# Kernel optimization log

Measured on AMD Instinct MI355X. Metric: run time of the kernel, lower is better.

## Reference

```python
import jax, jax.numpy as jnp
import numpy as np

L, B, T, E, H, V = 6, 4, 1024, 768, 12, 32000
FF = 4 * E


def setup_inputs() -> dict:
    key = jax.random.key(0)
    ks = jax.random.split(key, 16)
    n = lambda k, shape: jax.random.normal(k, shape, jnp.float32) * 0.02
    return {
        "idx": jax.random.randint(ks[0], (B, T), 0, V),
        "targets": jax.random.randint(ks[1], (B, T), 0, V),
        "tok_emb": n(ks[2], (V, E)),
        "pos_emb": n(ks[3], (T, E)),  # block_size == T
        "Wq": n(ks[4], (L, E, E)),
        "Wk": n(ks[5], (L, E, E)),
        "Wv": n(ks[6], (L, E, E)),
        "Wp": n(ks[7], (L, E, E)),
        "bp": jnp.zeros((L, E), jnp.float32),
        "W1": n(ks[8], (L, E, FF)),
        "b1": jnp.zeros((L, FF), jnp.float32),
        "W2": n(ks[9], (L, FF, E)),
        "b2": jnp.zeros((L, E), jnp.float32),
        "ln1_g": jnp.ones((L, E), jnp.float32),
        "ln1_b": jnp.zeros((L, E), jnp.float32),
        "ln2_g": jnp.ones((L, E), jnp.float32),
        "ln2_b": jnp.zeros((L, E), jnp.float32),
        "lnf_g": jnp.ones((E,), jnp.float32),
        "lnf_b": jnp.zeros((E,), jnp.float32),
        "Wlm": n(ks[10], (E, V)),
        "blm": jnp.zeros((V,), jnp.float32),
    }


def _ln(x, g, b):
    m = jnp.mean(x, -1, keepdims=True)
    v = jnp.var(x, -1, keepdims=True)
    return (x - m) * jax.lax.rsqrt(v + 1e-5) * g + b


def _attn(x, wq, wk, wv, wp, pb):
    b, t, e = x.shape
    hs = e // H
    q = (x @ wq).reshape(b, t, H, hs).transpose(0, 2, 1, 3)
    k = (x @ wk).reshape(b, t, H, hs).transpose(0, 2, 1, 3)
    v = (x @ wv).reshape(b, t, H, hs).transpose(0, 2, 1, 3)
    s = jnp.einsum('bhqd,bhkd->bhqk', q, k) * (hs ** -0.5)
    mask = jnp.tril(jnp.ones((t, t), bool))
    s = jnp.where(mask, s, -jnp.inf)
    p = jax.nn.softmax(s, axis=-1)  # dropout = identity at eval
    o = jnp.einsum('bhqk,bhkd->bhqd', p, v).transpose(0, 2, 1, 3).reshape(b, t, e)
    return o @ wp + pb


def reference(idx, targets, tok_emb, pos_emb, Wq, Wk, Wv, Wp, bp, W1, b1, W2, b2,
              ln1_g, ln1_b, ln2_g, ln2_b, lnf_g, lnf_b, Wlm, blm):
    x = tok_emb[idx] + pos_emb[:idx.shape[1]]

    def step(x, p):
        wq, wk, wv, wp, pb, w1, pb1, w2, pb2, g1, bb1, g2, bb2 = p
        x = x + _attn(_ln(x, g1, bb1), wq, wk, wv, wp, pb)
        h = _ln(x, g2, bb2)
        x = x + (jax.nn.relu(h @ w1 + pb1) @ w2 + pb2)
        return x, None

    x, _ = jax.lax.scan(step, x, (Wq, Wk, Wv, Wp, bp, W1, b1, W2, b2,
                                  ln1_g, ln1_b, ln2_g, ln2_b))
    x = _ln(x, lnf_g, lnf_b)
    logits = x @ Wlm + blm
    logp = jax.nn.log_softmax(logits, axis=-1)
    loss = -jnp.mean(jnp.take_along_axis(logp, targets[..., None], axis=-1))
    return logits, loss
```

## Files before the change

kernel.cpp:

```cpp
#include <hip/hip_runtime.h>
#include <hip/hip_bf16.h>
#include <math.h>

#define LAYERS 6
#define BB 4
#define TT 1024
#define EE 768
#define HH 12
#define HS 64
#define VV 32000
#define FFD 3072
#define MROWS (BB * TT)
#define QS (3 * EE)
#define KVB 64
#define QBLK 128
#define NPART (VV / 256)

typedef __attribute__((ext_vector_type(8))) short bf16x8_t;
typedef __attribute__((ext_vector_type(4))) float f32x4_t;

__device__ __forceinline__ float wave_sum(float v) {
#pragma unroll
    for (int o = 32; o > 0; o >>= 1) v += __shfl_xor(v, o);
    return v;
}
__device__ __forceinline__ float wave_max(float v) {
#pragma unroll
    for (int o = 32; o > 0; o >>= 1) v = fmaxf(v, __shfl_xor(v, o));
    return v;
}
__device__ __forceinline__ float block_sum256(float v, float* red) {
    v = wave_sum(v);
    int tid = threadIdx.x;
    if ((tid & 63) == 0) red[tid >> 6] = v;
    __syncthreads();
    float r = red[0] + red[1] + red[2] + red[3];
    __syncthreads();
    return r;
}
__device__ __forceinline__ float block_max256(float v, float* red) {
    v = wave_max(v);
    int tid = threadIdx.x;
    if ((tid & 63) == 0) red[tid >> 6] = v;
    __syncthreads();
    float r = fmaxf(fmaxf(red[0], red[1]), fmaxf(red[2], red[3]));
    __syncthreads();
    return r;
}

__device__ __forceinline__ void gload_lds16(const void* g, void* l) {
    __builtin_amdgcn_global_load_lds((const __attribute__((address_space(1))) void*)g,
                                     (__attribute__((address_space(3))) void*)l, 16, 0, 0);
}

__device__ __forceinline__ unsigned pk2bf(float lo, float hi) {
    __hip_bfloat162 h2 = __float22bfloat162_rn(make_float2(lo, hi));
    return *reinterpret_cast<unsigned*>(&h2);
}

__global__ __launch_bounds__(256) void embed_k(const int* __restrict__ idx,
                                               const float* __restrict__ tok,
                                               const float* __restrict__ pos,
                                               float* __restrict__ x) {
    int row = blockIdx.x;
    int t = row & (TT - 1);
    int token = idx[row];
    const float* te = tok + (size_t)token * EE;
    const float* pe = pos + (size_t)t * EE;
    float* xr = x + (size_t)row * EE;
    for (int i = threadIdx.x; i < EE; i += 256) xr[i] = te[i] + pe[i];
}

__global__ __launch_bounds__(256) void ln_k(const float* __restrict__ x,
                                            const float* __restrict__ g,
                                            const float* __restrict__ b,
                                            __hip_bfloat16* __restrict__ out) {
    __shared__ float sr[EE];
    __shared__ float red[4];
    int row = blockIdx.x;
    const float* xr = x + (size_t)row * EE;
    int tid = threadIdx.x;
    float s = 0.f;
    for (int i = tid; i < EE; i += 256) { float v = xr[i]; sr[i] = v; s += v; }
    s = block_sum256(s, red);
    float m = s * (1.0f / EE);
    float vs = 0.f;
    for (int i = tid; i < EE; i += 256) { float d = sr[i] - m; vs += d * d; }
    vs = block_sum256(vs, red);
    float rstd = rsqrtf(vs * (1.0f / EE) + 1e-5f);
    __hip_bfloat16* orow = out + (size_t)row * EE;
    for (int i = tid; i < EE; i += 256)
        orow[i] = __float2bfloat16((sr[i] - m) * rstd * g[i] + b[i]);
}

__global__ __launch_bounds__(256) void tconv_b_k(const float* __restrict__ W,
                                                 __hip_bfloat16* __restrict__ WT,
                                                 int R, int C,
                                                 size_t wstride, size_t tstride) {
    __shared__ float t[32][33];
    const float* Wl = W + (size_t)blockIdx.z * wstride;
    __hip_bfloat16* Tl = WT + (size_t)blockIdx.z * tstride;
    int c0 = blockIdx.x * 32, r0 = blockIdx.y * 32;
    int tx = threadIdx.x & 31, ty = threadIdx.x >> 5;
#pragma unroll
    for (int i = 0; i < 4; ++i)
        t[ty + 8 * i][tx] = Wl[(size_t)(r0 + ty + 8 * i) * C + c0 + tx];
    __syncthreads();
#pragma unroll
    for (int i = 0; i < 4; ++i)
        Tl[(size_t)(c0 + ty + 8 * i) * R + r0 + tx] = __float2bfloat16(t[tx][ty + 8 * i]);
}

template <bool BIAS, bool RELU, bool ACCUM, bool OBF16>
__global__ __launch_bounds__(256) void mgemm_k(const __hip_bfloat16* __restrict__ A,
                                               const __hip_bfloat16* __restrict__ BT,
                                               const float* __restrict__ bias,
                                               void* __restrict__ Cv,
                                               int M, int N, int K, int ntn) {
    __shared__ __align__(16) short As[128 * 32];
    __shared__ __align__(16) short Bs[128 * 32];

    int nwg = gridDim.x;
    int bid = blockIdx.x;
    int cpx = nwg >> 3;
    int swz = (bid & 7) * cpx + (bid >> 3);
    int tm = swz / ntn, tn = swz - tm * ntn;
    int m0 = tm * 128, n0 = tn * 128;

    int tid = threadIdx.x;
    int lane = tid & 63;
    int wave = tid >> 6;
    int wr = wave >> 1, wc = wave & 1;

    f32x4_t acc[4][4];
#pragma unroll
    for (int i = 0; i < 4; ++i)
#pragma unroll
        for (int j = 0; j < 4; ++j)
#pragma unroll
            for (int r = 0; r < 4; ++r) acc[i][j][r] = 0.f;

    const short* Ag = (const short*)A;
    const short* Bg = (const short*)BT;
    const int arow0 = tid >> 2;
    const int arow1 = (tid + 256) >> 2;
    const int acol = (tid & 3) * 8;

    const int fr = lane & 15;
    const int kg = (lane >> 4) * 8;

    for (int k0 = 0; k0 < K; k0 += 32) {
        gload_lds16(Ag + (size_t)(m0 + arow0) * K + k0 + acol, &As[tid * 8]);
        gload_lds16(Ag + (size_t)(m0 + arow1) * K + k0 + acol, &As[(tid + 256) * 8]);
        gload_lds16(Bg + (size_t)(n0 + arow0) * K + k0 + acol, &Bs[tid * 8]);
        gload_lds16(Bg + (size_t)(n0 + arow1) * K + k0 + acol, &Bs[(tid + 256) * 8]);
        __syncthreads();

        bf16x8_t af[4], bq[4];
#pragma unroll
        for (int mi = 0; mi < 4; ++mi)
            af[mi] = *(const bf16x8_t*)&As[(wr * 64 + mi * 16 + fr) * 32 + kg];
#pragma unroll
        for (int ni = 0; ni < 4; ++ni)
            bq[ni] = *(const bf16x8_t*)&Bs[(wc * 64 + ni * 16 + fr) * 32 + kg];
#pragma unroll
        for (int mi = 0; mi < 4; ++mi)
#pragma unroll
            for (int ni = 0; ni < 4; ++ni)
                acc[mi][ni] = __builtin_amdgcn_mfma_f32_16x16x32_bf16(af[mi], bq[ni], acc[mi][ni], 0, 0, 0);
        __syncthreads();
    }

    float bvec[4];
    if (BIAS) {
#pragma unroll
        for (int ni = 0; ni < 4; ++ni) bvec[ni] = bias[n0 + wc * 64 + ni * 16 + fr];
    }
    const int rbase = m0 + wr * 64 + (lane >> 4) * 4;
    const int cbase = n0 + wc * 64 + fr;
#pragma unroll
    for (int mi = 0; mi < 4; ++mi) {
#pragma unroll
        for (int ni = 0; ni < 4; ++ni) {
#pragma unroll
            for (int r = 0; r < 4; ++r) {
                int row = rbase + mi * 16 + r;
                int col = cbase + ni * 16;
                float v = acc[mi][ni][r];
                if (BIAS) v += bvec[ni];
                if (RELU) v = fmaxf(v, 0.f);
                size_t off = (size_t)row * N + col;
                if (OBF16) {
                    ((__hip_bfloat16*)Cv)[off] = __float2bfloat16(v);
                } else {
                    float* Cf = (float*)Cv;
                    if (ACCUM) Cf[off] += v; else Cf[off] = v;
                }
            }
        }
    }
}

__device__ __forceinline__ bf16x8_t ldsrd256(const short* base, int row, int colb) {
    return *(const bf16x8_t*)((const char*)base + ((row << 7) + (colb ^ ((row & 7) << 4))));
}

template <bool BIAS, bool RELU, bool OBF16, bool LSE>
__global__ __launch_bounds__(512, 2) void mgemm256_k(const __hip_bfloat16* __restrict__ A,
                                                     const __hip_bfloat16* __restrict__ BT,
                                                     const float* __restrict__ bias,
                                                     void* __restrict__ Cv,
                                                     int M, int N, int K,
                                                     int ntn, int npart,
                                                     float2* __restrict__ partials) {
    __shared__ __align__(16) short lds[2][2][2][8192];

    const int nwg = gridDim.x;
    const int bid = blockIdx.x;
    const int cpx = nwg >> 3;
    const int swz = (bid & 7) * cpx + (bid >> 3);
    const int tm = swz / ntn, tn = swz - tm * ntn;
    const int m0 = tm * 256, n0 = tn * 256;

    const int tid = threadIdx.x;
    const int lane = tid & 63;
    const int wave = tid >> 6;
    const int wm = wave >> 2;
    const int wn = wave & 3;
    const int fr = lane & 15;
    const int hi4 = lane >> 4;

    const short* Ag = (const short*)A;
    const short* Bg = (const short*)BT;
    const int nt = K >> 6;

    auto stage_half = [&](const short* g, int grow0, int k0, short* lbase) {
#pragma unroll
        for (int sub = 0; sub < 2; ++sub) {
            int d = sub * 8192 + tid * 16;
            int row = d >> 7;
            int cb = d & 127;
            int col = (cb ^ ((row & 7) << 4)) >> 1;
            gload_lds16(g + (size_t)(grow0 + row) * K + k0 + col, (char*)lbase + d);
        }
    };

    f32x4_t acc[2][2][4][2];
#pragma unroll
    for (int ah = 0; ah < 2; ++ah)
#pragma unroll
        for (int s = 0; s < 2; ++s)
#pragma unroll
            for (int mi = 0; mi < 4; ++mi)
#pragma unroll
                for (int ni = 0; ni < 2; ++ni)
#pragma unroll
                    for (int r = 0; r < 4; ++r) acc[ah][s][mi][ni][r] = 0.f;

    stage_half(Ag, m0 + 0,   0,  &lds[0][0][0][0]);
    stage_half(Bg, n0 + 0,   0,  &lds[0][1][0][0]);
    stage_half(Ag, m0 + 128, 0,  &lds[0][0][1][0]);
    stage_half(Bg, n0 + 128, 0,  &lds[0][1][1][0]);
    stage_half(Ag, m0 + 0,   64, &lds[1][0][0][0]);
    stage_half(Bg, n0 + 0,   64, &lds[1][1][0][0]);
    asm volatile("s_waitcnt vmcnt(4)" ::: "memory");
    __builtin_amdgcn_s_barrier();

    for (int t = 0; t < nt; ++t) {
        const int c = t & 1, o = c ^ 1;
        bf16x8_t a[4][2];
#pragma unroll
        for (int p = 0; p < 4; ++p) {
            const int ah = p >> 1, s = p & 1;
            if (s == 0) {
#pragma unroll
                for (int mi = 0; mi < 4; ++mi)
#pragma unroll
                    for (int kk = 0; kk < 2; ++kk)
                        a[mi][kk] = ldsrd256(&lds[c][0][ah][0],
                                             wm * 64 + mi * 16 + fr, kk * 64 + hi4 * 16);
            }
            bf16x8_t b[2][2];
#pragma unroll
            for (int ni = 0; ni < 2; ++ni)
#pragma unroll
                for (int kk = 0; kk < 2; ++kk)
                    b[ni][kk] = ldsrd256(&lds[c][1][s][0],
                                         wn * 32 + ni * 16 + fr, kk * 64 + hi4 * 16);
            if (p == 0 && t + 1 < nt) stage_half(Ag, m0 + 128, (t + 1) * 64, &lds[o][0][1][0]);
            if (p == 1 && t + 1 < nt) stage_half(Bg, n0 + 128, (t + 1) * 64, &lds[o][1][1][0]);
            if (p == 2 && t + 2 < nt) stage_half(Ag, m0 + 0,   (t + 2) * 64, &lds[c][0][0][0]);
            if (p == 3 && t + 2 < nt) stage_half(Bg, n0 + 0,   (t + 2) * 64, &lds[c][1][0][0]);
            if (p == 3) {
                if (t < nt - 2)       asm volatile("s_waitcnt vmcnt(4)" ::: "memory");
                else if (t == nt - 2) asm volatile("s_waitcnt vmcnt(0)" ::: "memory");
            }
            __builtin_amdgcn_s_barrier();
            asm volatile("s_waitcnt lgkmcnt(0)" ::: "memory");
            __builtin_amdgcn_sched_barrier(0);
            __builtin_amdgcn_s_setprio(1);
#pragma unroll
            for (int mi = 0; mi < 4; ++mi)
#pragma unroll
                for (int ni = 0; ni < 2; ++ni)
#pragma unroll
                    for (int kk = 0; kk < 2; ++kk)
                        acc[ah][s][mi][ni] = __builtin_amdgcn_mfma_f32_16x16x32_bf16(
                            a[mi][kk], b[ni][kk], acc[ah][s][mi][ni], 0, 0, 0);
            __builtin_amdgcn_s_setprio(0);
            __builtin_amdgcn_s_barrier();
        }
    }

    float bv[2][2];
    if (BIAS) {
#pragma unroll
        for (int s = 0; s < 2; ++s)
#pragma unroll
            for (int ni = 0; ni < 2; ++ni)
                bv[s][ni] = bias[n0 + s * 128 + wn * 32 + ni * 16 + fr];
    }
    float2* red = (float2*)&lds[0][0][0][0];
#pragma unroll
    for (int ah = 0; ah < 2; ++ah) {
#pragma unroll
        for (int mi = 0; mi < 4; ++mi) {
#pragma unroll
            for (int r = 0; r < 4; ++r) {
                const int rb = ah * 128 + wm * 64 + mi * 16 + hi4 * 4 + r;
                const size_t grow = (size_t)(m0 + rb);
                float v[2][2];
#pragma unroll
                for (int s = 0; s < 2; ++s)
#pragma unroll
                    for (int ni = 0; ni < 2; ++ni) {
                        float vv = acc[ah][s][mi][ni][r];
                        if (BIAS) vv += bv[s][ni];
                        if (RELU) vv = fmaxf(vv, 0.f);
                        v[s][ni] = vv;
                        size_t off = grow * N + n0 + s * 128 + wn * 32 + ni * 16 + fr;
                        if (OBF16) ((__hip_bfloat16*)Cv)[off] = __float2bfloat16(vv);
                        else       ((float*)Cv)[off] = vv;
                    }
                if (LSE) {
                    float mx = fmaxf(fmaxf(v[0][0], v[0][1]), fmaxf(v[1][0], v[1][1]));
#pragma unroll
                    for (int off2 = 1; off2 < 16; off2 <<= 1) mx = fmaxf(mx, __shfl_xor(mx, off2));
                    float sm = 0.f;
#pragma unroll
                    for (int s = 0; s < 2; ++s)
#pragma unroll
                        for (int ni = 0; ni < 2; ++ni) sm += __expf(v[s][ni] - mx);
#pragma unroll
                    for (int off2 = 1; off2 < 16; off2 <<= 1) sm += __shfl_xor(sm, off2);
                    if (fr == 0) red[rb * 4 + wn] = make_float2(mx, sm);
                }
            }
        }
    }
    if (LSE) {
        __syncthreads();
        if (tid < 256) {
            float2 p0 = red[tid * 4 + 0], p1 = red[tid * 4 + 1];
            float2 p2 = red[tid * 4 + 2], p3 = red[tid * 4 + 3];
            float M2 = fmaxf(fmaxf(p0.x, p1.x), fmaxf(p2.x, p3.x));
            float L2 = p0.y * __expf(p0.x - M2) + p1.y * __expf(p1.x - M2) +
                       p2.y * __expf(p2.x - M2) + p3.y * __expf(p3.x - M2);
            partials[(size_t)(m0 + tid) * npart + tn] = make_float2(M2, L2);
        }
    }
}

__global__ __launch_bounds__(256) void fattn_k(const __hip_bfloat16* __restrict__ qkv,
                                               __hip_bfloat16* __restrict__ o) {
    __shared__ short Ks[KVB * HS];
    __shared__ short Vt[HS * KVB];
    __shared__ short Pl[4 * 32 * KVB];

    const int bh = blockIdx.x;
    const int hh = bh % HH;
    const int bI = bh / HH;
    const int qt = (TT / QBLK - 1) - blockIdx.y;
    const int q0 = qt * QBLK;

    const int tid = threadIdx.x;
    const int lane = tid & 63;
    const int wave = tid >> 6;
    const int fr = lane & 15;
    const int hi4 = lane >> 4;

    const size_t rowbase = (size_t)bI * TT;
    const int wq0 = q0 + wave * 32;

    bf16x8_t qf[2][2];
#pragma unroll
    for (int mi = 0; mi < 2; ++mi)
#pragma unroll
        for (int kc = 0; kc < 2; ++kc) {
            const short* src = (const short*)qkv +
                (rowbase + wq0 + mi * 16 + fr) * QS + hh * HS + kc * 32 + hi4 * 8;
            bf16x8_t v = *(const bf16x8_t*)src;
#pragma unroll
            for (int e = 0; e < 8; ++e) {
                float f = __uint_as_float(((unsigned)(unsigned short)v[e]) << 16) * 0.125f;
                v[e] = (short)(__float_as_uint(f) >> 16);
            }
            qf[mi][kc] = v;
        }

    f32x4_t oa[2][4];
    float m_r[2], l_r[2];
#pragma unroll
    for (int mi = 0; mi < 2; ++mi) {
        m_r[mi] = -INFINITY;
        l_r[mi] = 0.f;
#pragma unroll
        for (int nd = 0; nd < 4; ++nd)
#pragma unroll
            for (int r = 0; r < 4; ++r) oa[mi][nd][r] = 0.f;
    }

    const int skey = tid >> 2;
    const int sd0 = (tid & 3) * 16;
    const int niter = 2 * (qt + 1);

    for (int it = 0; it < niter; ++it) {
        const int kv0 = it * KVB;
        __syncthreads();
        {
            const short* kg = (const short*)qkv + (rowbase + kv0 + skey) * QS + EE + hh * HS + sd0;
            uint4 ka = *(const uint4*)kg;
            uint4 kb2 = *(const uint4*)(kg + 8);
            const int rs = (skey & 7) << 4;
            char* kbp = (char*)Ks;
            *(uint4*)(kbp + ((skey * 128 + sd0 * 2) ^ rs)) = ka;
            *(uint4*)(kbp + ((skey * 128 + sd0 * 2 + 16) ^ rs)) = kb2;

            const short* vg = (const short*)qkv + (rowbase + kv0 + skey) * QS + 2 * EE + hh * HS + sd0;
            uint4 va = *(const uint4*)vg;
            uint4 vb2 = *(const uint4*)(vg + 8);
            char* vbp = (char*)Vt;
            const short* vs0 = (const short*)&va;
#pragma unroll
            for (int e = 0; e < 8; ++e) {
                int dd = sd0 + e;
                *(short*)(vbp + ((dd * 128 + skey * 2) ^ ((dd & 7) << 4))) = vs0[e];
            }
            const short* vs1 = (const short*)&vb2;
#pragma unroll
            for (int e = 0; e < 8; ++e) {
                int dd = sd0 + 8 + e;
                *(short*)(vbp + ((dd * 128 + skey * 2) ^ ((dd & 7) << 4))) = vs1[e];
            }
        }
        __syncthreads();

        f32x4_t sa[2][4];
#pragma unroll
        for (int mi = 0; mi < 2; ++mi)
#pragma unroll
            for (int ni = 0; ni < 4; ++ni)
#pragma unroll
                for (int r = 0; r < 4; ++r) sa[mi][ni][r] = 0.f;
#pragma unroll
        for (int kc = 0; kc < 2; ++kc) {
            bf16x8_t kf[4];
#pragma unroll
            for (int ni = 0; ni < 4; ++ni) {
                int krow = ni * 16 + fr;
                kf[ni] = *(const bf16x8_t*)((char*)Ks +
                    ((krow * 128 + (kc * 32 + hi4 * 8) * 2) ^ ((krow & 7) << 4)));
            }
#pragma unroll
            for (int mi = 0; mi < 2; ++mi)
#pragma unroll
                for (int ni = 0; ni < 4; ++ni)
                    sa[mi][ni] = __builtin_amdgcn_mfma_f32_16x16x32_bf16(kf[ni], qf[mi][kc], sa[mi][ni], 0, 0, 0);
        }

        if (kv0 + KVB - 1 > wq0) {
#pragma unroll
            for (int mi = 0; mi < 2; ++mi) {
                int qrow = wq0 + mi * 16 + fr;
#pragma unroll
                for (int ni = 0; ni < 4; ++ni)
#pragma unroll
                    for (int r = 0; r < 4; ++r) {
                        int key = kv0 + ni * 16 + hi4 * 4 + r;
                        if (key > qrow) sa[mi][ni][r] = -1e30f;
                    }
            }
        }

        char* Pw = (char*)Pl + wave * 4096;
#pragma unroll
        for (int mi = 0; mi < 2; ++mi) {
            float mx = sa[mi][0][0];
#pragma unroll
            for (int ni = 0; ni < 4; ++ni)
#pragma unroll
                for (int r = 0; r < 4; ++r) mx = fmaxf(mx, sa[mi][ni][r]);
            mx = fmaxf(mx, __shfl_xor(mx, 16));
            mx = fmaxf(mx, __shfl_xor(mx, 32));
            float mnew = fmaxf(m_r[mi], mx);
            float al = __expf(m_r[mi] - mnew);
            m_r[mi] = mnew;
            float ps = 0.f;
#pragma unroll
            for (int ni = 0; ni < 4; ++ni) {
#pragma unroll
                for (int r = 0; r < 4; ++r) {
                    float p = __expf(sa[mi][ni][r] - mnew);
                    sa[mi][ni][r] = p;
                    ps += p;
                }
                uint2 pw;
                pw.x = pk2bf(sa[mi][ni][0], sa[mi][ni][1]);
                pw.y = pk2bf(sa[mi][ni][2], sa[mi][ni][3]);
                int prow = mi * 16 + fr;
                int cb = ni * 32 + hi4 * 8;
                *(uint2*)(Pw + ((prow * 128 + cb) ^ ((prow & 7) << 4))) = pw;
            }
            ps += __shfl_xor(ps, 16);
            ps += __shfl_xor(ps, 32);
            l_r[mi] = l_r[mi] * al + ps;
#pragma unroll
            for (int r = 0; r < 4; ++r) {
                float a_r = __shfl(al, hi4 * 4 + r);
#pragma unroll
                for (int nd = 0; nd < 4; ++nd) oa[mi][nd][r] *= a_r;
            }
        }

#pragma unroll
        for (int kc = 0; kc < 2; ++kc) {
            bf16x8_t pf[2], vf[4];
#pragma unroll
            for (int mi = 0; mi < 2; ++mi) {
                int prow = mi * 16 + fr;
                pf[mi] = *(const bf16x8_t*)(Pw +
                    ((prow * 128 + (kc * 32 + hi4 * 8) * 2) ^ ((prow & 7) << 4)));
            }
#pragma unroll
            for (int nd = 0; nd < 4; ++nd) {
                int vrow = nd * 16 + fr;
                vf[nd] = *(const bf16x8_t*)((char*)Vt +
                    ((vrow * 128 + (kc * 32 + hi4 * 8) * 2) ^ ((vrow & 7) << 4)));
            }
#pragma unroll
            for (int mi = 0; mi < 2; ++mi)
#pragma unroll
                for (int nd = 0; nd < 4; ++nd)
                    oa[mi][nd] = __builtin_amdgcn_mfma_f32_16x16x32_bf16(pf[mi], vf[nd], oa[mi][nd], 0, 0, 0);
        }
    }

#pragma unroll
    for (int mi = 0; mi < 2; ++mi)
#pragma unroll
        for (int r = 0; r < 4; ++r) {
            float lr = __shfl(l_r[mi], hi4 * 4 + r);
            float inv = 1.0f / lr;
            int row = wq0 + mi * 16 + hi4 * 4 + r;
            __hip_bfloat16* orow = o + (rowbase + row) * EE + hh * HS;
#pragma unroll
            for (int nd = 0; nd < 4; ++nd)
                orow[nd * 16 + fr] = __float2bfloat16(oa[mi][nd][r] * inv);
        }
}

__global__ __launch_bounds__(256) void rowloss2_k(const float2* __restrict__ partials,
                                                  const float* __restrict__ logits,
                                                  const int* __restrict__ targets,
                                                  float* __restrict__ rowloss, int ntn) {
    __shared__ float red[4];
    int row = blockIdx.x;
    int tid = threadIdx.x;
    float m = -INFINITY, l = 0.f;
    if (tid < ntn) {
        float2 p = partials[(size_t)row * ntn + tid];
        m = p.x; l = p.y;
    }
    float mg = block_max256(m, red);
    float s = (tid < ntn) ? l * __expf(m - mg) : 0.f;
    s = block_sum256(s, red);
    if (tid == 0)
        rowloss[row] = mg + logf(s) - logits[(size_t)row * VV + targets[row]];
}

__global__ __launch_bounds__(256) void loss_final_k(const float* __restrict__ rowloss,
                                                    float* __restrict__ out) {
    __shared__ float red[4];
    float s = 0.f;
    for (int i = threadIdx.x; i < MROWS; i += 256) s += rowloss[i];
    s = block_sum256(s, red);
    if (threadIdx.x == 0) out[0] = s * (1.0f / MROWS);
}

extern "C" void kernel_launch(void* const* d_in, const int* in_sizes, int n_in,
                              void* d_out, int out_size, void* d_ws, size_t ws_size,
                              hipStream_t stream) {
    const int* idx      = (const int*)d_in[0];
    const int* targets  = (const int*)d_in[1];
    const float* tok    = (const float*)d_in[2];
    const float* pos    = (const float*)d_in[3];
    const float* Wq     = (const float*)d_in[4];
    const float* Wk     = (const float*)d_in[5];
    const float* Wv     = (const float*)d_in[6];
    const float* Wp     = (const float*)d_in[7];
    const float* bp     = (const float*)d_in[8];
    const float* W1     = (const float*)d_in[9];
    const float* b1     = (const float*)d_in[10];
    const float* W2     = (const float*)d_in[11];
    const float* b2     = (const float*)d_in[12];
    const float* ln1_g  = (const float*)d_in[13];
    const float* ln1_b  = (const float*)d_in[14];
    const float* ln2_g  = (const float*)d_in[15];
    const float* ln2_b  = (const float*)d_in[16];
    const float* lnf_g  = (const float*)d_in[17];
    const float* lnf_b  = (const float*)d_in[18];
    const float* Wlm    = (const float*)d_in[19];
    const float* blm    = (const float*)d_in[20];

    float* out = (float*)d_out;

    char* w = (char*)d_ws;
    float* x = (float*)w;                             w += (size_t)MROWS * EE * 4;
    __hip_bfloat16* hbf = (__hip_bfloat16*)w;         w += (size_t)MROWS * EE * 2;
    __hip_bfloat16* qkv = (__hip_bfloat16*)w;         w += (size_t)MROWS * QS * 2;
    __hip_bfloat16* obf = (__hip_bfloat16*)w;         w += (size_t)MROWS * EE * 2;
    __hip_bfloat16* ff1 = (__hip_bfloat16*)w;         w += (size_t)MROWS * FFD * 2;
    float2* partials = (float2*)ff1;
    __hip_bfloat16* wlmT = (__hip_bfloat16*)w;        w += (size_t)VV * EE * 2;
    float* rowloss = (float*)w;                       w += (size_t)MROWS * 4 + 256;
    __hip_bfloat16* wbase = (__hip_bfloat16*)w;

    const size_t base_used = (size_t)(w - (char*)d_ws);
    const size_t per_layer_w = ((size_t)QS * EE + (size_t)EE * EE +
                                (size_t)FFD * EE + (size_t)EE * FFD) * 2;
    const bool hoist = ws_size >= base_used + per_layer_w * LAYERS;
    const int nlw = hoist ? LAYERS : 1;

    __hip_bfloat16* qkvwT = wbase;
    __hip_bfloat16* wpT   = qkvwT + (size_t)nlw * QS * EE;
    __hip_bfloat16* w1T   = wpT   + (size_t)nlw * EE * EE;
    __hip_bfloat16* w2T   = w1T   + (size_t)nlw * FFD * EE;

    dim3 blk(256);

    embed_k<<<MROWS, blk, 0, stream>>>(idx, tok, pos, x);

    if (hoist) {
        tconv_b_k<<<dim3(EE / 32, EE / 32, LAYERS), blk, 0, stream>>>(
            Wq, qkvwT, EE, EE, (size_t)EE * EE, (size_t)QS * EE);
        tconv_b_k<<<dim3(EE / 32, EE / 32, LAYERS), blk, 0, stream>>>(
            Wk, qkvwT + (size_t)EE * EE, EE, EE, (size_t)EE * EE, (size_t)QS * EE);
        tconv_b_k<<<dim3(EE / 32, EE / 32, LAYERS), blk, 0, stream>>>(
            Wv, qkvwT + (size_t)2 * EE * EE, EE, EE, (size_t)EE * EE, (size_t)QS * EE);
        tconv_b_k<<<dim3(EE / 32, EE / 32, LAYERS), blk, 0, stream>>>(
            Wp, wpT, EE, EE, (size_t)EE * EE, (size_t)EE * EE);
        tconv_b_k<<<dim3(FFD / 32, EE / 32, LAYERS), blk, 0, stream>>>(
            W1, w1T, EE, FFD, (size_t)EE * FFD, (size_t)FFD * EE);
        tconv_b_k<<<dim3(EE / 32, FFD / 32, LAYERS), blk, 0, stream>>>(
            W2, w2T, FFD, EE, (size_t)FFD * EE, (size_t)EE * FFD);
    }
    tconv_b_k<<<dim3(VV / 32, EE / 32, 1), blk, 0, stream>>>(Wlm, wlmT, EE, VV, 0, 0);

    for (int l = 0; l < LAYERS; ++l) {
        __hip_bfloat16* qkvwT_l = qkvwT + (hoist ? (size_t)l * QS * EE : 0);
        __hip_bfloat16* wpT_l   = wpT   + (hoist ? (size_t)l * EE * EE : 0);
        __hip_bfloat16* w1T_l   = w1T   + (hoist ? (size_t)l * FFD * EE : 0);
        __hip_bfloat16* w2T_l   = w2T   + (hoist ? (size_t)l * EE * FFD : 0);
        if (!hoist) {
            tconv_b_k<<<dim3(EE / 32, EE / 32, 1), blk, 0, stream>>>(
                Wq + (size_t)l * EE * EE, qkvwT_l, EE, EE, 0, 0);
            tconv_b_k<<<dim3(EE / 32, EE / 32, 1), blk, 0, stream>>>(
                Wk + (size_t)l * EE * EE, qkvwT_l + (size_t)EE * EE, EE, EE, 0, 0);
            tconv_b_k<<<dim3(EE / 32, EE / 32, 1), blk, 0, stream>>>(
                Wv + (size_t)l * EE * EE, qkvwT_l + (size_t)2 * EE * EE, EE, EE, 0, 0);
            tconv_b_k<<<dim3(EE / 32, EE / 32, 1), blk, 0, stream>>>(
                Wp + (size_t)l * EE * EE, wpT_l, EE, EE, 0, 0);
            tconv_b_k<<<dim3(FFD / 32, EE / 32, 1), blk, 0, stream>>>(
                W1 + (size_t)l * EE * FFD, w1T_l, EE, FFD, 0, 0);
            tconv_b_k<<<dim3(EE / 32, FFD / 32, 1), blk, 0, stream>>>(
                W2 + (size_t)l * FFD * EE, w2T_l, FFD, EE, 0, 0);
        }

        ln_k<<<MROWS, blk, 0, stream>>>(x, ln1_g + l * EE, ln1_b + l * EE, hbf);
        mgemm_k<false, false, false, true><<<dim3((MROWS / 128) * (QS / 128)), blk, 0, stream>>>(
            hbf, qkvwT_l, nullptr, qkv, MROWS, QS, EE, QS / 128);
        fattn_k<<<dim3(BB * HH, TT / QBLK), blk, 0, stream>>>(qkv, obf);
        mgemm_k<true, false, true, false><<<dim3((MROWS / 128) * (EE / 128)), blk, 0, stream>>>(
            obf, wpT_l, bp + l * EE, x, MROWS, EE, EE, EE / 128);
        ln_k<<<MROWS, blk, 0, stream>>>(x, ln2_g + l * EE, ln2_b + l * EE, hbf);
        mgemm_k<true, true, false, true><<<dim3((MROWS / 128) * (FFD / 128)), blk, 0, stream>>>(
            hbf, w1T_l, b1 + l * FFD, ff1, MROWS, FFD, EE, FFD / 128);
        mgemm_k<true, false, true, false><<<dim3((MROWS / 128) * (EE / 128)), blk, 0, stream>>>(
            ff1, w2T_l, b2 + l * EE, x, MROWS, EE, FFD, EE / 128);
    }

    ln_k<<<MROWS, blk, 0, stream>>>(x, lnf_g, lnf_b, hbf);
    mgemm256_k<true, false, false, true><<<dim3((MROWS / 256) * (VV / 256)), dim3(512), 0, stream>>>(
        hbf, wlmT, blm, out, MROWS, VV, EE, VV / 256, NPART, partials);

    rowloss2_k<<<MROWS, blk, 0, stream>>>(partials, out, targets, rowloss, NPART);
    loss_final_k<<<1, blk, 0, stream>>>(rowloss, out + (size_t)MROWS * VV);
}
```

Baseline: 1.850 ms.

## Vectorize embed/layernorm, simplify LM-head GEMM tiling, prefetch K/V in attention

Embedding and layernorm now process four rows per block, one wave per row, with float4 loads and wave-level reductions instead of block reductions through LDS. The LM-head GEMM is replaced by a simpler 128x256 tile kernel with a single LDS buffer and a K step of 32 per barrier pair. It drops the hand-pipelined double buffering and the 256x256 tile in exchange for higher occupancy (launch bounds of 4 blocks per unit). Flash attention now register-prefetches the next K/V tile while computing the current one, hiding global load latency. The LM-head change risks losing the previous software pipelining on the largest GEMM.

```diff
diff --git a/kernel.cpp b/kernel.cpp
--- a/kernel.cpp
+++ b/kernel.cpp
@@ -58,39 +58,62 @@
     return *reinterpret_cast<unsigned*>(&h2);
 }
 
-__global__ __launch_bounds__(256) void embed_k(const int* __restrict__ idx,
-                                               const float* __restrict__ tok,
-                                               const float* __restrict__ pos,
-                                               float* __restrict__ x) {
-    int row = blockIdx.x;
+__global__ __launch_bounds__(256) void embed4_k(const int* __restrict__ idx,
+                                                const float* __restrict__ tok,
+                                                const float* __restrict__ pos,
+                                                float* __restrict__ x) {
+    int row = blockIdx.x * 4 + (threadIdx.x >> 6);
+    int lane = threadIdx.x & 63;
     int t = row & (TT - 1);
     int token = idx[row];
-    const float* te = tok + (size_t)token * EE;
-    const float* pe = pos + (size_t)t * EE;
-    float* xr = x + (size_t)row * EE;
-    for (int i = threadIdx.x; i < EE; i += 256) xr[i] = te[i] + pe[i];
-}
-
-__global__ __launch_bounds__(256) void ln_k(const float* __restrict__ x,
-                                            const float* __restrict__ g,
-                                            const float* __restrict__ b,
-                                            __hip_bfloat16* __restrict__ out) {
-    __shared__ float sr[EE];
-    __shared__ float red[4];
-    int row = blockIdx.x;
-    const float* xr = x + (size_t)row * EE;
-    int tid = threadIdx.x;
+    const float4* te = (const float4*)(tok + (size_t)token * EE);
+    const float4* pe = (const float4*)(pos + (size_t)t * EE);
+    float4* xr = (float4*)(x + (size_t)row * EE);
+#pragma unroll
+    for (int j = 0; j < 3; ++j) {
+        int i = j * 64 + lane;
+        float4 a = te[i], b = pe[i];
+        xr[i] = make_float4(a.x + b.x, a.y + b.y, a.z + b.z, a.w + b.w);
+    }
+}
+
+__global__ __launch_bounds__(256) void ln4_k(const float* __restrict__ x,
+                                             const float* __restrict__ g,
+                                             const float* __restrict__ b,
+                                             __hip_bfloat16* __restrict__ out) {
+    int row = blockIdx.x * 4 + (threadIdx.x >> 6);
+    int lane = threadIdx.x & 63;
+    const float4* xr = (const float4*)(x + (size_t)row * EE);
+    float4 v[3];
     float s = 0.f;
-    for (int i = tid; i < EE; i += 256) { float v = xr[i]; sr[i] = v; s += v; }
-    s = block_sum256(s, red);
+#pragma unroll
+    for (int j = 0; j < 3; ++j) {
+        v[j] = xr[j * 64 + lane];
+        s += v[j].x + v[j].y + v[j].z + v[j].w;
+    }
+    s = wave_sum(s);
     float m = s * (1.0f / EE);
     float vs = 0.f;
-    for (int i = tid; i < EE; i += 256) { float d = sr[i] - m; vs += d * d; }
-    vs = block_sum256(vs, red);
+#pragma unroll
+    for (int j = 0; j < 3; ++j) {
+        float d0 = v[j].x - m, d1 = v[j].y - m, d2 = v[j].z - m, d3 = v[j].w - m;
+        vs += d0 * d0 + d1 * d1 + d2 * d2 + d3 * d3;
+    }
+    vs = wave_sum(vs);
     float rstd = rsqrtf(vs * (1.0f / EE) + 1e-5f);
-    __hip_bfloat16* orow = out + (size_t)row * EE;
-    for (int i = tid; i < EE; i += 256)
-        orow[i] = __float2bfloat16((sr[i] - m) * rstd * g[i] + b[i]);
+    const float4* g4 = (const float4*)g;
+    const float4* b4 = (const float4*)b;
+    uint2* orow = (uint2*)(out + (size_t)row * EE);
+#pragma unroll
+    for (int j = 0; j < 3; ++j) {
+        int i = j * 64 + lane;
+        float4 gg = g4[i], bb = b4[i];
+        float n0 = (v[j].x - m) * rstd * gg.x + bb.x;
+        float n1 = (v[j].y - m) * rstd * gg.y + bb.y;
+        float n2 = (v[j].z - m) * rstd * gg.z + bb.z;
+        float n3 = (v[j].w - m) * rstd * gg.w + bb.w;
+        orow[i] = make_uint2(pk2bf(n0, n1), pk2bf(n2, n3));
+    }
 }
 
 __global__ __launch_bounds__(256) void tconv_b_k(const float* __restrict__ W,
@@ -201,26 +224,22 @@
     }
 }
 
-__device__ __forceinline__ bf16x8_t ldsrd256(const short* base, int row, int colb) {
-    return *(const bf16x8_t*)((const char*)base + ((row << 7) + (colb ^ ((row & 7) << 4))));
-}
-
-template <bool BIAS, bool RELU, bool OBF16, bool LSE>
-__global__ __launch_bounds__(512, 2) void mgemm256_k(const __hip_bfloat16* __restrict__ A,
+__global__ __launch_bounds__(512, 4) void mgemm_lm_k(const __hip_bfloat16* __restrict__ A,
                                                      const __hip_bfloat16* __restrict__ BT,
                                                      const float* __restrict__ bias,
-                                                     void* __restrict__ Cv,
+                                                     float* __restrict__ C,
                                                      int M, int N, int K,
                                                      int ntn, int npart,
                                                      float2* __restrict__ partials) {
-    __shared__ __align__(16) short lds[2][2][2][8192];
+    __shared__ __align__(16) short As[128 * 32];
+    __shared__ __align__(16) short Bs[256 * 32];
 
     const int nwg = gridDim.x;
     const int bid = blockIdx.x;
     const int cpx = nwg >> 3;
     const int swz = (bid & 7) * cpx + (bid >> 3);
     const int tm = swz / ntn, tn = swz - tm * ntn;
-    const int m0 = tm * 256, n0 = tn * 256;
+    const int m0 = tm * 128, n0 = tn * 256;
 
     const int tid = threadIdx.x;
     const int lane = tid & 63;
@@ -230,144 +249,79 @@
     const int fr = lane & 15;
     const int hi4 = lane >> 4;
 
+    f32x4_t acc[4][4];
+#pragma unroll
+    for (int i = 0; i < 4; ++i)
+#pragma unroll
+        for (int j = 0; j < 4; ++j)
+#pragma unroll
+            for (int r = 0; r < 4; ++r) acc[i][j][r] = 0.f;
+
     const short* Ag = (const short*)A;
     const short* Bg = (const short*)BT;
-    const int nt = K >> 6;
-
-    auto stage_half = [&](const short* g, int grow0, int k0, short* lbase) {
-#pragma unroll
-        for (int sub = 0; sub < 2; ++sub) {
-            int d = sub * 8192 + tid * 16;
-            int row = d >> 7;
-            int cb = d & 127;
-            int col = (cb ^ ((row & 7) << 4)) >> 1;
-            gload_lds16(g + (size_t)(grow0 + row) * K + k0 + col, (char*)lbase + d);
-        }
-    };
-
-    f32x4_t acc[2][2][4][2];
-#pragma unroll
-    for (int ah = 0; ah < 2; ++ah)
-#pragma unroll
-        for (int s = 0; s < 2; ++s)
-#pragma unroll
-            for (int mi = 0; mi < 4; ++mi)
-#pragma unroll
-                for (int ni = 0; ni < 2; ++ni)
-#pragma unroll
-                    for (int r = 0; r < 4; ++r) acc[ah][s][mi][ni][r] = 0.f;
-
-    stage_half(Ag, m0 + 0,   0,  &lds[0][0][0][0]);
-    stage_half(Bg, n0 + 0,   0,  &lds[0][1][0][0]);
-    stage_half(Ag, m0 + 128, 0,  &lds[0][0][1][0]);
-    stage_half(Bg, n0 + 128, 0,  &lds[0][1][1][0]);
-    stage_half(Ag, m0 + 0,   64, &lds[1][0][0][0]);
-    stage_half(Bg, n0 + 0,   64, &lds[1][1][0][0]);
-    asm volatile("s_waitcnt vmcnt(4)" ::: "memory");
-    __builtin_amdgcn_s_barrier();
-
-    for (int t = 0; t < nt; ++t) {
-        const int c = t & 1, o = c ^ 1;
-        bf16x8_t a[4][2];
-#pragma unroll
-        for (int p = 0; p < 4; ++p) {
-            const int ah = p >> 1, s = p & 1;
-            if (s == 0) {
-#pragma unroll
-                for (int mi = 0; mi < 4; ++mi)
-#pragma unroll
-                    for (int kk = 0; kk < 2; ++kk)
-                        a[mi][kk] = ldsrd256(&lds[c][0][ah][0],
-                                             wm * 64 + mi * 16 + fr, kk * 64 + hi4 * 16);
-            }
-            bf16x8_t b[2][2];
-#pragma unroll
-            for (int ni = 0; ni < 2; ++ni)
-#pragma unroll
-                for (int kk = 0; kk < 2; ++kk)
-                    b[ni][kk] = ldsrd256(&lds[c][1][s][0],
-                                         wn * 32 + ni * 16 + fr, kk * 64 + hi4 * 16);
-            if (p == 0 && t + 1 < nt) stage_half(Ag, m0 + 128, (t + 1) * 64, &lds[o][0][1][0]);
-            if (p == 1 && t + 1 < nt) stage_half(Bg, n0 + 128, (t + 1) * 64, &lds[o][1][1][0]);
-            if (p == 2 && t + 2 < nt) stage_half(Ag, m0 + 0,   (t + 2) * 64, &lds[c][0][0][0]);
-            if (p == 3 && t + 2 < nt) stage_half(Bg, n0 + 0,   (t + 2) * 64, &lds[c][1][0][0]);
-            if (p == 3) {
-                if (t < nt - 2)       asm volatile("s_waitcnt vmcnt(4)" ::: "memory");
-                else if (t == nt - 2) asm volatile("s_waitcnt vmcnt(0)" ::: "memory");
-            }
-            __builtin_amdgcn_s_barrier();
-            asm volatile("s_waitcnt lgkmcnt(0)" ::: "memory");
-            __builtin_amdgcn_sched_barrier(0);
-            __builtin_amdgcn_s_setprio(1);
-#pragma unroll
-            for (int mi = 0; mi < 4; ++mi)
-#pragma unroll
-                for (int ni = 0; ni < 2; ++ni)
-#pragma unroll
-                    for (int kk = 0; kk < 2; ++kk)
-                        acc[ah][s][mi][ni] = __builtin_amdgcn_mfma_f32_16x16x32_bf16(
-                            a[mi][kk], b[ni][kk], acc[ah][s][mi][ni], 0, 0, 0);
-            __builtin_amdgcn_s_setprio(0);
-            __builtin_amdgcn_s_barrier();
-        }
-    }
-
-    float bv[2][2];
-    if (BIAS) {
-#pragma unroll
-        for (int s = 0; s < 2; ++s)
-#pragma unroll
-            for (int ni = 0; ni < 2; ++ni)
-                bv[s][ni] = bias[n0 + s * 128 + wn * 32 + ni * 16 + fr];
-    }
-    float2* red = (float2*)&lds[0][0][0][0];
-#pragma unroll
-    for (int ah = 0; ah < 2; ++ah) {
-#pragma unroll
-        for (int mi = 0; mi < 4; ++mi) {
-#pragma unroll
-            for (int r = 0; r < 4; ++r) {
-                const int rb = ah * 128 + wm * 64 + mi * 16 + hi4 * 4 + r;
-                const size_t grow = (size_t)(m0 + rb);
-                float v[2][2];
-#pragma unroll
-                for (int s = 0; s < 2; ++s)
-#pragma unroll
-                    for (int ni = 0; ni < 2; ++ni) {
-                        float vv = acc[ah][s][mi][ni][r];
-                        if (BIAS) vv += bv[s][ni];
-                        if (RELU) vv = fmaxf(vv, 0.f);
-                        v[s][ni] = vv;
-                        size_t off = grow * N + n0 + s * 128 + wn * 32 + ni * 16 + fr;
-                        if (OBF16) ((__hip_bfloat16*)Cv)[off] = __float2bfloat16(vv);
-                        else       ((float*)Cv)[off] = vv;
-                    }
-                if (LSE) {
-                    float mx = fmaxf(fmaxf(v[0][0], v[0][1]), fmaxf(v[1][0], v[1][1]));
-#pragma unroll
-                    for (int off2 = 1; off2 < 16; off2 <<= 1) mx = fmaxf(mx, __shfl_xor(mx, off2));
-                    float sm = 0.f;
-#pragma unroll
-                    for (int s = 0; s < 2; ++s)
-#pragma unroll
-                        for (int ni = 0; ni < 2; ++ni) sm += __expf(v[s][ni] - mx);
-#pragma unroll
-                    for (int off2 = 1; off2 < 16; off2 <<= 1) sm += __shfl_xor(sm, off2);
-                    if (fr == 0) red[rb * 4 + wn] = make_float2(mx, sm);
-                }
-            }
-        }
-    }
-    if (LSE) {
+    const int srow = tid >> 2;
+    const int scol = (tid & 3) * 8;
+    const int kg = hi4 * 8;
+
+    for (int k0 = 0; k0 < K; k0 += 32) {
+        gload_lds16(Ag + (size_t)(m0 + srow) * K + k0 + scol, &As[tid * 8]);
+        gload_lds16(Bg + (size_t)(n0 + srow) * K + k0 + scol, &Bs[tid * 8]);
+        gload_lds16(Bg + (size_t)(n0 + 128 + srow) * K + k0 + scol, &Bs[(tid + 512) * 8]);
         __syncthreads();
-        if (tid < 256) {
-            float2 p0 = red[tid * 4 + 0], p1 = red[tid * 4 + 1];
-            float2 p2 = red[tid * 4 + 2], p3 = red[tid * 4 + 3];
-            float M2 = fmaxf(fmaxf(p0.x, p1.x), fmaxf(p2.x, p3.x));
-            float L2 = p0.y * __expf(p0.x - M2) + p1.y * __expf(p1.x - M2) +
-                       p2.y * __expf(p2.x - M2) + p3.y * __expf(p3.x - M2);
-            partials[(size_t)(m0 + tid) * npart + tn] = make_float2(M2, L2);
-        }
+
+        bf16x8_t af[4], bq[4];
+#pragma unroll
+        for (int mi = 0; mi < 4; ++mi)
+            af[mi] = *(const bf16x8_t*)&As[(wm * 64 + mi * 16 + fr) * 32 + kg];
+#pragma unroll
+        for (int ni = 0; ni < 4; ++ni)
+            bq[ni] = *(const bf16x8_t*)&Bs[(wn * 64 + ni * 16 + fr) * 32 + kg];
+#pragma unroll
+        for (int mi = 0; mi < 4; ++mi)
+#pragma unroll
+            for (int ni = 0; ni < 4; ++ni)
+                acc[mi][ni] = __builtin_amdgcn_mfma_f32_16x16x32_bf16(af[mi], bq[ni], acc[mi][ni], 0, 0, 0);
+        __syncthreads();
+    }
+
+    float bvec[4];
+#pragma unroll
+    for (int ni = 0; ni < 4; ++ni) bvec[ni] = bias[n0 + wn * 64 + ni * 16 + fr];
+
+    float2* red = (float2*)As;
+    const int cbase = n0 + wn * 64 + fr;
+#pragma unroll
+    for (int mi = 0; mi < 4; ++mi) {
+#pragma unroll
+        for (int r = 0; r < 4; ++r) {
+            const int rl = wm * 64 + mi * 16 + hi4 * 4 + r;
+            const size_t grow = (size_t)(m0 + rl);
+            float v4[4];
+#pragma unroll
+            for (int ni = 0; ni < 4; ++ni) {
+                float v = acc[mi][ni][r] + bvec[ni];
+                v4[ni] = v;
+                C[grow * N + cbase + ni * 16] = v;
+            }
+            float mx = fmaxf(fmaxf(v4[0], v4[1]), fmaxf(v4[2], v4[3]));
+#pragma unroll
+            for (int o = 1; o < 16; o <<= 1) mx = fmaxf(mx, __shfl_xor(mx, o));
+            float sm = 0.f;
+#pragma unroll
+            for (int ni = 0; ni < 4; ++ni) sm += __expf(v4[ni] - mx);
+#pragma unroll
+            for (int o = 1; o < 16; o <<= 1) sm += __shfl_xor(sm, o);
+            if (fr == 0) red[rl * 4 + wn] = make_float2(mx, sm);
+        }
+    }
+    __syncthreads();
+    if (tid < 128) {
+        float2 p0 = red[tid * 4 + 0], p1 = red[tid * 4 + 1];
+        float2 p2 = red[tid * 4 + 2], p3 = red[tid * 4 + 3];
+        float M2 = fmaxf(fmaxf(p0.x, p1.x), fmaxf(p2.x, p3.x));
+        float L2 = p0.y * __expf(p0.x - M2) + p1.y * __expf(p1.x - M2) +
+                   p2.y * __expf(p2.x - M2) + p3.y * __expf(p3.x - M2);
+        partials[(size_t)(m0 + tid) * npart + tn] = make_float2(M2, L2);
     }
 }
 
@@ -424,21 +378,22 @@
     const int sd0 = (tid & 3) * 16;
     const int niter = 2 * (qt + 1);
 
+    uint4 ka, kb2, va, vb2;
+    {
+        const short* kg = (const short*)qkv + (rowbase + skey) * QS + EE + hh * HS + sd0;
+        ka = *(const uint4*)kg; kb2 = *(const uint4*)(kg + 8);
+        const short* vg = (const short*)qkv + (rowbase + skey) * QS + 2 * EE + hh * HS + sd0;
+        va = *(const uint4*)vg; vb2 = *(const uint4*)(vg + 8);
+    }
+
     for (int it = 0; it < niter; ++it) {
-        const int kv0 = it * KVB;
         __syncthreads();
         {
-            const short* kg = (const short*)qkv + (rowbase + kv0 + skey) * QS + EE + hh * HS + sd0;
-            uint4 ka = *(const uint4*)kg;
-            uint4 kb2 = *(const uint4*)(kg + 8);
             const int rs = (skey & 7) << 4;
             char* kbp = (char*)Ks;
             *(uint4*)(kbp + ((skey * 128 + sd0 * 2) ^ rs)) = ka;
             *(uint4*)(kbp + ((skey * 128 + sd0 * 2 + 16) ^ rs)) = kb2;
 
-            const short* vg = (const short*)qkv + (rowbase + kv0 + skey) * QS + 2 * EE + hh * HS + sd0;
-            uint4 va = *(const uint4*)vg;
-            uint4 vb2 = *(const uint4*)(vg + 8);
             char* vbp = (char*)Vt;
             const short* vs0 = (const short*)&va;
 #pragma unroll
@@ -454,6 +409,16 @@
             }
         }
         __syncthreads();
+
+        if (it + 1 < niter) {
+            const int kvn = (it + 1) * KVB;
+            const short* kg = (const short*)qkv + (rowbase + kvn + skey) * QS + EE + hh * HS + sd0;
+            ka = *(const uint4*)kg; kb2 = *(const uint4*)(kg + 8);
+            const short* vg = (const short*)qkv + (rowbase + kvn + skey) * QS + 2 * EE + hh * HS + sd0;
+            va = *(const uint4*)vg; vb2 = *(const uint4*)(vg + 8);
+        }
+
+        const int kv0 = it * KVB;
 
         f32x4_t sa[2][4];
 #pragma unroll
@@ -648,7 +613,7 @@
 
     dim3 blk(256);
 
-    embed_k<<<MROWS, blk, 0, stream>>>(idx, tok, pos, x);
+    embed4_k<<<MROWS / 4, blk, 0, stream>>>(idx, tok, pos, x);
 
     if (hoist) {
         tconv_b_k<<<dim3(EE / 32, EE / 32, LAYERS), blk, 0, stream>>>(
@@ -686,21 +651,21 @@
                 W2 + (size_t)l * FFD * EE, w2T_l, FFD, EE, 0, 0);
         }
 
-        ln_k<<<MROWS, blk, 0, stream>>>(x, ln1_g + l * EE, ln1_b + l * EE, hbf);
+        ln4_k<<<MROWS / 4, blk, 0, stream>>>(x, ln1_g + l * EE, ln1_b + l * EE, hbf);
         mgemm_k<false, false, false, true><<<dim3((MROWS / 128) * (QS / 128)), blk, 0, stream>>>(
             hbf, qkvwT_l, nullptr, qkv, MROWS, QS, EE, QS / 128);
         fattn_k<<<dim3(BB * HH, TT / QBLK), blk, 0, stream>>>(qkv, obf);
         mgemm_k<true, false, true, false><<<dim3((MROWS / 128) * (EE / 128)), blk, 0, stream>>>(
             obf, wpT_l, bp + l * EE, x, MROWS, EE, EE, EE / 128);
-        ln_k<<<MROWS, blk, 0, stream>>>(x, ln2_g + l * EE, ln2_b + l * EE, hbf);
+        ln4_k<<<MROWS / 4, blk, 0, stream>>>(x, ln2_g + l * EE, ln2_b + l * EE, hbf);
         mgemm_k<true, true, false, true><<<dim3((MROWS / 128) * (FFD / 128)), blk, 0, stream>>>(
             hbf, w1T_l, b1 + l * FFD, ff1, MROWS, FFD, EE, FFD / 128);
         mgemm_k<true, false, true, false><<<dim3((MROWS / 128) * (EE / 128)), blk, 0, stream>>>(
             ff1, w2T_l, b2 + l * EE, x, MROWS, EE, FFD, EE / 128);
     }
 
-    ln_k<<<MROWS, blk, 0, stream>>>(x, lnf_g, lnf_b, hbf);
-    mgemm256_k<true, false, false, true><<<dim3((MROWS / 256) * (VV / 256)), dim3(512), 0, stream>>>(
+    ln4_k<<<MROWS / 4, blk, 0, stream>>>(x, lnf_g, lnf_b, hbf);
+    mgemm_lm_k<<<dim3((MROWS / 128) * (VV / 256)), dim3(512), 0, stream>>>(
         hbf, wlmT, blm, out, MROWS, VV, EE, VV / 256, NPART, partials);
 
     rowloss2_k<<<MROWS, blk, 0, stream>>>(partials, out, targets, rowloss, NPART);
```

Measured after the change: 1.823 ms. No clear change (-1.4%).

## Vectorize LN/embed per-wave, shrink M tile for N=768 GEMMs, prefetch attention KV

Applied to the files above, without the earlier changes.

Layernorm and embedding now process one row per wave with float4 loads and wave-level reductions instead of one row per 256-thread block, which drops shared-memory round trips and block syncs. The GEMM gains an MI template parameter, and the two N=768 projections use 64-row tiles so the grid doubles and fills more CUs. The flash-attention loop register-prefetches the next K/V tile while computing on the current one. These are several unrelated changes, and they add register pressure in the attention kernel.

```diff
diff --git a/kernel.cpp b/kernel.cpp
--- a/kernel.cpp
+++ b/kernel.cpp
@@ -58,39 +58,62 @@
     return *reinterpret_cast<unsigned*>(&h2);
 }
 
-__global__ __launch_bounds__(256) void embed_k(const int* __restrict__ idx,
-                                               const float* __restrict__ tok,
-                                               const float* __restrict__ pos,
-                                               float* __restrict__ x) {
-    int row = blockIdx.x;
+__global__ __launch_bounds__(256) void embed4_k(const int* __restrict__ idx,
+                                                const float* __restrict__ tok,
+                                                const float* __restrict__ pos,
+                                                float* __restrict__ x) {
+    int row = blockIdx.x * 4 + (threadIdx.x >> 6);
+    int lane = threadIdx.x & 63;
     int t = row & (TT - 1);
     int token = idx[row];
-    const float* te = tok + (size_t)token * EE;
-    const float* pe = pos + (size_t)t * EE;
-    float* xr = x + (size_t)row * EE;
-    for (int i = threadIdx.x; i < EE; i += 256) xr[i] = te[i] + pe[i];
-}
-
-__global__ __launch_bounds__(256) void ln_k(const float* __restrict__ x,
-                                            const float* __restrict__ g,
-                                            const float* __restrict__ b,
-                                            __hip_bfloat16* __restrict__ out) {
-    __shared__ float sr[EE];
-    __shared__ float red[4];
-    int row = blockIdx.x;
-    const float* xr = x + (size_t)row * EE;
-    int tid = threadIdx.x;
+    const float4* te = (const float4*)(tok + (size_t)token * EE);
+    const float4* pe = (const float4*)(pos + (size_t)t * EE);
+    float4* xr = (float4*)(x + (size_t)row * EE);
+#pragma unroll
+    for (int j = 0; j < 3; ++j) {
+        int i = j * 64 + lane;
+        float4 a = te[i], b = pe[i];
+        xr[i] = make_float4(a.x + b.x, a.y + b.y, a.z + b.z, a.w + b.w);
+    }
+}
+
+__global__ __launch_bounds__(256) void ln4_k(const float* __restrict__ x,
+                                             const float* __restrict__ g,
+                                             const float* __restrict__ b,
+                                             __hip_bfloat16* __restrict__ out) {
+    int row = blockIdx.x * 4 + (threadIdx.x >> 6);
+    int lane = threadIdx.x & 63;
+    const float4* xr = (const float4*)(x + (size_t)row * EE);
+    float4 v[3];
     float s = 0.f;
-    for (int i = tid; i < EE; i += 256) { float v = xr[i]; sr[i] = v; s += v; }
-    s = block_sum256(s, red);
+#pragma unroll
+    for (int j = 0; j < 3; ++j) {
+        v[j] = xr[j * 64 + lane];
+        s += v[j].x + v[j].y + v[j].z + v[j].w;
+    }
+    s = wave_sum(s);
     float m = s * (1.0f / EE);
     float vs = 0.f;
-    for (int i = tid; i < EE; i += 256) { float d = sr[i] - m; vs += d * d; }
-    vs = block_sum256(vs, red);
+#pragma unroll
+    for (int j = 0; j < 3; ++j) {
+        float d0 = v[j].x - m, d1 = v[j].y - m, d2 = v[j].z - m, d3 = v[j].w - m;
+        vs += d0 * d0 + d1 * d1 + d2 * d2 + d3 * d3;
+    }
+    vs = wave_sum(vs);
     float rstd = rsqrtf(vs * (1.0f / EE) + 1e-5f);
-    __hip_bfloat16* orow = out + (size_t)row * EE;
-    for (int i = tid; i < EE; i += 256)
-        orow[i] = __float2bfloat16((sr[i] - m) * rstd * g[i] + b[i]);
+    const float4* g4 = (const float4*)g;
+    const float4* b4 = (const float4*)b;
+    uint2* orow = (uint2*)(out + (size_t)row * EE);
+#pragma unroll
+    for (int j = 0; j < 3; ++j) {
+        int i = j * 64 + lane;
+        float4 gg = g4[i], bb = b4[i];
+        float n0 = (v[j].x - m) * rstd * gg.x + bb.x;
+        float n1 = (v[j].y - m) * rstd * gg.y + bb.y;
+        float n2 = (v[j].z - m) * rstd * gg.z + bb.z;
+        float n3 = (v[j].w - m) * rstd * gg.w + bb.w;
+        orow[i] = make_uint2(pk2bf(n0, n1), pk2bf(n2, n3));
+    }
 }
 
 __global__ __launch_bounds__(256) void tconv_b_k(const float* __restrict__ W,
@@ -111,13 +134,13 @@
         Tl[(size_t)(c0 + ty + 8 * i) * R + r0 + tx] = __float2bfloat16(t[tx][ty + 8 * i]);
 }
 
-template <bool BIAS, bool RELU, bool ACCUM, bool OBF16>
+template <bool BIAS, bool RELU, bool ACCUM, bool OBF16, int MI>
 __global__ __launch_bounds__(256) void mgemm_k(const __hip_bfloat16* __restrict__ A,
                                                const __hip_bfloat16* __restrict__ BT,
                                                const float* __restrict__ bias,
                                                void* __restrict__ Cv,
                                                int M, int N, int K, int ntn) {
-    __shared__ __align__(16) short As[128 * 32];
+    __shared__ __align__(16) short As[MI * 32 * 32];
     __shared__ __align__(16) short Bs[128 * 32];
 
     int nwg = gridDim.x;
@@ -125,16 +148,16 @@
     int cpx = nwg >> 3;
     int swz = (bid & 7) * cpx + (bid >> 3);
     int tm = swz / ntn, tn = swz - tm * ntn;
-    int m0 = tm * 128, n0 = tn * 128;
+    int m0 = tm * (MI * 32), n0 = tn * 128;
 
     int tid = threadIdx.x;
     int lane = tid & 63;
     int wave = tid >> 6;
     int wr = wave >> 1, wc = wave & 1;
 
-    f32x4_t acc[4][4];
-#pragma unroll
-    for (int i = 0; i < 4; ++i)
+    f32x4_t acc[MI][4];
+#pragma unroll
+    for (int i = 0; i < MI; ++i)
 #pragma unroll
         for (int j = 0; j < 4; ++j)
 #pragma unroll
@@ -151,20 +174,21 @@
 
     for (int k0 = 0; k0 < K; k0 += 32) {
         gload_lds16(Ag + (size_t)(m0 + arow0) * K + k0 + acol, &As[tid * 8]);
-        gload_lds16(Ag + (size_t)(m0 + arow1) * K + k0 + acol, &As[(tid + 256) * 8]);
+        if (MI == 4)
+            gload_lds16(Ag + (size_t)(m0 + arow1) * K + k0 + acol, &As[(tid + 256) * 8]);
         gload_lds16(Bg + (size_t)(n0 + arow0) * K + k0 + acol, &Bs[tid * 8]);
         gload_lds16(Bg + (size_t)(n0 + arow1) * K + k0 + acol, &Bs[(tid + 256) * 8]);
         __syncthreads();
 
-        bf16x8_t af[4], bq[4];
-#pragma unroll
-        for (int mi = 0; mi < 4; ++mi)
-            af[mi] = *(const bf16x8_t*)&As[(wr * 64 + mi * 16 + fr) * 32 + kg];
+        bf16x8_t af[MI], bq[4];
+#pragma unroll
+        for (int mi = 0; mi < MI; ++mi)
+            af[mi] = *(const bf16x8_t*)&As[(wr * (MI * 16) + mi * 16 + fr) * 32 + kg];
 #pragma unroll
         for (int ni = 0; ni < 4; ++ni)
             bq[ni] = *(const bf16x8_t*)&Bs[(wc * 64 + ni * 16 + fr) * 32 + kg];
 #pragma unroll
-        for (int mi = 0; mi < 4; ++mi)
+        for (int mi = 0; mi < MI; ++mi)
 #pragma unroll
             for (int ni = 0; ni < 4; ++ni)
                 acc[mi][ni] = __builtin_amdgcn_mfma_f32_16x16x32_bf16(af[mi], bq[ni], acc[mi][ni], 0, 0, 0);
@@ -176,10 +200,10 @@
 #pragma unroll
         for (int ni = 0; ni < 4; ++ni) bvec[ni] = bias[n0 + wc * 64 + ni * 16 + fr];
     }
-    const int rbase = m0 + wr * 64 + (lane >> 4) * 4;
+    const int rbase = m0 + wr * (MI * 16) + (lane >> 4) * 4;
     const int cbase = n0 + wc * 64 + fr;
 #pragma unroll
-    for (int mi = 0; mi < 4; ++mi) {
+    for (int mi = 0; mi < MI; ++mi) {
 #pragma unroll
         for (int ni = 0; ni < 4; ++ni) {
 #pragma unroll
@@ -424,21 +448,22 @@
     const int sd0 = (tid & 3) * 16;
     const int niter = 2 * (qt + 1);
 
+    uint4 ka, kb2, va, vb2;
+    {
+        const short* kg = (const short*)qkv + (rowbase + skey) * QS + EE + hh * HS + sd0;
+        ka = *(const uint4*)kg; kb2 = *(const uint4*)(kg + 8);
+        const short* vg = (const short*)qkv + (rowbase + skey) * QS + 2 * EE + hh * HS + sd0;
+        va = *(const uint4*)vg; vb2 = *(const uint4*)(vg + 8);
+    }
+
     for (int it = 0; it < niter; ++it) {
-        const int kv0 = it * KVB;
         __syncthreads();
         {
-            const short* kg = (const short*)qkv + (rowbase + kv0 + skey) * QS + EE + hh * HS + sd0;
-            uint4 ka = *(const uint4*)kg;
-            uint4 kb2 = *(const uint4*)(kg + 8);
             const int rs = (skey & 7) << 4;
             char* kbp = (char*)Ks;
             *(uint4*)(kbp + ((skey * 128 + sd0 * 2) ^ rs)) = ka;
             *(uint4*)(kbp + ((skey * 128 + sd0 * 2 + 16) ^ rs)) = kb2;
 
-            const short* vg = (const short*)qkv + (rowbase + kv0 + skey) * QS + 2 * EE + hh * HS + sd0;
-            uint4 va = *(const uint4*)vg;
-            uint4 vb2 = *(const uint4*)(vg + 8);
             char* vbp = (char*)Vt;
             const short* vs0 = (const short*)&va;
 #pragma unroll
@@ -454,6 +479,16 @@
             }
         }
         __syncthreads();
+
+        if (it + 1 < niter) {
+            const int kvn = (it + 1) * KVB;
+            const short* kg = (const short*)qkv + (rowbase + kvn + skey) * QS + EE + hh * HS + sd0;
+            ka = *(const uint4*)kg; kb2 = *(const uint4*)(kg + 8);
+            const short* vg = (const short*)qkv + (rowbase + kvn + skey) * QS + 2 * EE + hh * HS + sd0;
+            va = *(const uint4*)vg; vb2 = *(const uint4*)(vg + 8);
+        }
+
+        const int kv0 = it * KVB;
 
         f32x4_t sa[2][4];
 #pragma unroll
@@ -648,7 +683,7 @@
 
     dim3 blk(256);
 
-    embed_k<<<MROWS, blk, 0, stream>>>(idx, tok, pos, x);
+    embed4_k<<<MROWS / 4, blk, 0, stream>>>(idx, tok, pos, x);
 
     if (hoist) {
         tconv_b_k<<<dim3(EE / 32, EE / 32, LAYERS), blk, 0, stream>>>(
@@ -686,20 +721,20 @@
                 W2 + (size_t)l * FFD * EE, w2T_l, FFD, EE, 0, 0);
         }
 
-        ln_k<<<MROWS, blk, 0, stream>>>(x, ln1_g + l * EE, ln1_b + l * EE, hbf);
-        mgemm_k<false, false, false, true><<<dim3((MROWS / 128) * (QS / 128)), blk, 0, stream>>>(
+        ln4_k<<<MROWS / 4, blk, 0, stream>>>(x, ln1_g + l * EE, ln1_b + l * EE, hbf);
+        mgemm_k<false, false, false, true, 4><<<dim3((MROWS / 128) * (QS / 128)), blk, 0, stream>>>(
             hbf, qkvwT_l, nullptr, qkv, MROWS, QS, EE, QS / 128);
         fattn_k<<<dim3(BB * HH, TT / QBLK), blk, 0, stream>>>(qkv, obf);
-        mgemm_k<true, false, true, false><<<dim3((MROWS / 128) * (EE / 128)), blk, 0, stream>>>(
+        mgemm_k<true, false, true, false, 2><<<dim3((MROWS / 64) * (EE / 128)), blk, 0, stream>>>(
             obf, wpT_l, bp + l * EE, x, MROWS, EE, EE, EE / 128);
-        ln_k<<<MROWS, blk, 0, stream>>>(x, ln2_g + l * EE, ln2_b + l * EE, hbf);
-        mgemm_k<true, true, false, true><<<dim3((MROWS / 128) * (FFD / 128)), blk, 0, stream>>>(
+        ln4_k<<<MROWS / 4, blk, 0, stream>>>(x, ln2_g + l * EE, ln2_b + l * EE, hbf);
+        mgemm_k<true, true, false, true, 4><<<dim3((MROWS / 128) * (FFD / 128)), blk, 0, stream>>>(
             hbf, w1T_l, b1 + l * FFD, ff1, MROWS, FFD, EE, FFD / 128);
-        mgemm_k<true, false, true, false><<<dim3((MROWS / 128) * (EE / 128)), blk, 0, stream>>>(
+        mgemm_k<true, false, true, false, 2><<<dim3((MROWS / 64) * (EE / 128)), blk, 0, stream>>>(
             ff1, w2T_l, b2 + l * EE, x, MROWS, EE, FFD, EE / 128);
     }
 
-    ln_k<<<MROWS, blk, 0, stream>>>(x, lnf_g, lnf_b, hbf);
+    ln4_k<<<MROWS / 4, blk, 0, stream>>>(x, lnf_g, lnf_b, hbf);
     mgemm256_k<true, false, false, true><<<dim3((MROWS / 256) * (VV / 256)), dim3(512), 0, stream>>>(
         hbf, wlmT, blm, out, MROWS, VV, EE, VV / 256, NPART, partials);
 
```

Result: faster. 1.614 ms (-12.7%).
